# Performance work log

Hardware: AMD Instinct MI355X
Metric: run time of the kernel (lower is better)

The kernel has to match this reference:

```python
import jax, jax.numpy as jnp
import numpy as np

B, T, C = 4, 2048, 1024
H, HS = 16, 64  # n_heads, head_size; H*HS == C


def setup_inputs() -> dict:
    key = jax.random.key(0)
    ks = jax.random.split(key, 6)
    s = 0.02
    x = jax.random.normal(ks[0], (B, T, C), dtype=jnp.float32)
    Wq = jax.random.normal(ks[1], (H, C, HS), dtype=jnp.float32) * s
    Wk = jax.random.normal(ks[2], (H, C, HS), dtype=jnp.float32) * s
    Wv = jax.random.normal(ks[3], (H, C, HS), dtype=jnp.float32) * s
    Wo = jax.random.normal(ks[4], (C, C), dtype=jnp.float32) * s
    bo = jnp.zeros((C,), dtype=jnp.float32)
    return {"x": x, "Wq": Wq, "Wk": Wk, "Wv": Wv, "Wo": Wo, "bo": bo}


def reference(x, Wq, Wk, Wv, Wo, bo):
    # batched multi-head causal attention (math identical to per-head loop)
    q = jnp.einsum('btc,hcd->bhtd', x, Wq)  # [B,H,T,HS]
    k = jnp.einsum('btc,hcd->bhtd', x, Wk)
    v = jnp.einsum('btc,hcd->bhtd', x, Wv)
    scale = 1.0 / jnp.sqrt(jnp.asarray(HS, x.dtype))
    scores = jnp.einsum('bhtd,bhsd->bhts', q, k) * scale  # [B,H,T,T]
    causal = jnp.tril(jnp.ones((T, T), dtype=bool))
    scores = jnp.where(causal, scores, jnp.asarray(-jnp.inf, scores.dtype))
    attn = jax.nn.softmax(scores, axis=-1)
    out = jnp.einsum('bhts,bhsd->bhtd', attn, v)  # [B,H,T,HS]
    # concat heads along feature dim (head order == module list order)
    out = out.transpose(0, 2, 1, 3).reshape(B, T, C)
    return out @ Wo.T + bo
```

## Files before the change

### kernel.cpp

```cpp
#include <hip/hip_runtime.h>

typedef __attribute__((ext_vector_type(8))) short v8s;
typedef __attribute__((ext_vector_type(4))) short v4s;
typedef __attribute__((ext_vector_type(4))) float v4f;

static __device__ __forceinline__ short f2bf(float f) {
  union { float f; unsigned u; } c; c.f = f;
  unsigned r = c.u + 0x7fffu + ((c.u >> 16) & 1u);
  return (short)(r >> 16);
}

static __device__ __forceinline__ unsigned pk_bf16(float a, float b) {
  union { float f; unsigned u; } ca, cb; ca.f = a; cb.f = b;
  return ((ca.u + 0x8000u) >> 16) | ((cb.u + 0x8000u) & 0xffff0000u);
}

#if __has_builtin(__builtin_amdgcn_exp2f)
#define EXP2(x) __builtin_amdgcn_exp2f(x)
#else
#define EXP2(x) exp2f(x)
#endif

#define GLDS(gp, lp) __builtin_amdgcn_global_load_lds( \
    (const __attribute__((address_space(1))) void*)(gp), \
    (__attribute__((address_space(3))) void*)(lp), 16, 0, 0)


__global__ __launch_bounds__(256) void prep(const float* __restrict__ x,
                                            const float* __restrict__ Wq,
                                            const float* __restrict__ Wk,
                                            const float* __restrict__ Wv,
                                            const float* __restrict__ Wo,
                                            short* __restrict__ Xb,
                                            short* __restrict__ Wot,
                                            short* __restrict__ Wt) {
  __shared__ float tile[64][65];
  const int blk = blockIdx.x;
  const int tid = threadIdx.x;
  if (blk < 9216) {
    const float* src = (blk < 8192) ? x : Wo;
    short* dst = (blk < 8192) ? Xb : Wot;
    const int b2 = (blk < 8192) ? blk : (blk - 8192);
    const int idx = (b2 * 256 + tid) * 4;
    float4 v = *(const float4*)(src + idx);
    v4s o; o.x = f2bf(v.x); o.y = f2bf(v.y); o.z = f2bf(v.z); o.w = f2bf(v.w);
    *(v4s*)(dst + idx) = o;
    return;
  }
  const int bb = blk - 9216;
  const int sel = bb >> 8, rest = bb & 255;
  const int h = rest >> 4, kt = rest & 15;
  const float* W = (sel == 0) ? Wq : ((sel == 1) ? Wk : Wv);
  const int k0 = kt * 64;
  for (int i = 0; i < 4; ++i) {
    int c = i * 256 + tid;
    int row = c >> 4, c4 = (c & 15) * 4;
    float4 v = *(const float4*)(W + (size_t)h * 65536 + (size_t)(k0 + row) * 64 + c4);
    tile[row][c4 + 0] = v.x; tile[row][c4 + 1] = v.y;
    tile[row][c4 + 2] = v.z; tile[row][c4 + 3] = v.w;
  }
  __syncthreads();
  for (int i = 0; i < 2; ++i) {
    int c = i * 256 + tid;
    int d = c >> 3, k8 = (c & 7) * 8;
    v8s o;
    for (int j = 0; j < 8; ++j) o[j] = f2bf(tile[k8 + j][d]);
    *(v8s*)(Wt + (size_t)(sel * 1024 + h * 64 + d) * 1024 + k0 + k8) = o;
  }
}


#define GQ_STAGE_A(P, T) do {                                                     \
  _Pragma("unroll") for (int i_ = 0; i_ < 4; ++i_)                                \
    GLDS(Xb + (size_t)(m0 + rA + i_ * 64) * 1024 + (T) * 64 + cbl * 8,            \
         lds + (P) * 16384 + (tid + i_ * 512) * 8); } while (0)

#define GQ_STAGE_B(P, T) do {                                                     \
  _Pragma("unroll") for (int i_ = 0; i_ < 2; ++i_)                                \
    GLDS(Wt + (size_t)(n0 + rA + i_ * 64) * 1024 + (T) * 64 + cbl * 8,            \
         lds + 49152 + (P) * 8192 + (tid + i_ * 512) * 8); } while (0)

__global__ __launch_bounds__(512) void gemm_qkv(const short* __restrict__ Xb,
                                                const short* __restrict__ Wt,
                                                short* __restrict__ Qo,
                                                short* __restrict__ Ko,
                                                short* __restrict__ Vt) {
  __shared__ short lds[73728];
  const int tid = threadIdx.x;
  const int lane = tid & 63, quad = lane >> 4, l16 = lane & 15;
  const int wave = tid >> 6;
  const int m0 = blockIdx.x * 256, n0 = blockIdx.y * 128;
  const int wm = (wave >> 1) * 64, wn = (wave & 1) * 64;

  const int rA = tid >> 3;
  const int cbl = (tid & 7) ^ (rA & 7);

  const int swz = l16 & 7;
  const int csw0 = (quad ^ swz) * 8;
  const int csw1 = ((4 + quad) ^ swz) * 8;
  int aoff[4], boff[4];
#pragma unroll
  for (int mt = 0; mt < 4; ++mt) aoff[mt] = (wm + mt * 16 + l16) * 64;
#pragma unroll
  for (int nt = 0; nt < 4; ++nt) boff[nt] = (wn + nt * 16 + l16) * 64;

  v4f acc[4][4];
#pragma unroll
  for (int i = 0; i < 4; ++i)
#pragma unroll
    for (int j = 0; j < 4; ++j) acc[i][j] = (v4f){0.f, 0.f, 0.f, 0.f};

  GQ_STAGE_A(0, 0); GQ_STAGE_B(0, 0);
  GQ_STAGE_A(1, 1); GQ_STAGE_B(1, 1);
  asm volatile("s_waitcnt vmcnt(6)" ::: "memory");
  __builtin_amdgcn_s_barrier();

  int p = 0, pn = 2;
#pragma unroll 1
  for (int t = 0; t < 16; ++t) {
    int tn = t + 2; if (tn > 15) tn = 15;
    const short* lAp = lds + p * 16384;
    const short* lBp = lds + 49152 + p * 8192;

    GQ_STAGE_A(pn, tn);
    v8s a[4], b[4];
#pragma unroll
    for (int mt = 0; mt < 4; ++mt) a[mt] = *(const v8s*)(lAp + aoff[mt] + csw0);
#pragma unroll
    for (int nt = 0; nt < 4; ++nt) b[nt] = *(const v8s*)(lBp + boff[nt] + csw0);
    __builtin_amdgcn_s_setprio(1);
#pragma unroll
    for (int mt = 0; mt < 4; ++mt)
#pragma unroll
      for (int nt = 0; nt < 4; ++nt)
        acc[mt][nt] = __builtin_amdgcn_mfma_f32_16x16x32_bf16(a[mt], b[nt], acc[mt][nt], 0, 0, 0);
    __builtin_amdgcn_s_setprio(0);

    GQ_STAGE_B(pn, tn);
#pragma unroll
    for (int mt = 0; mt < 4; ++mt) a[mt] = *(const v8s*)(lAp + aoff[mt] + csw1);
#pragma unroll
    for (int nt = 0; nt < 4; ++nt) b[nt] = *(const v8s*)(lBp + boff[nt] + csw1);
    __builtin_amdgcn_s_setprio(1);
#pragma unroll
    for (int mt = 0; mt < 4; ++mt)
#pragma unroll
      for (int nt = 0; nt < 4; ++nt)
        acc[mt][nt] = __builtin_amdgcn_mfma_f32_16x16x32_bf16(a[mt], b[nt], acc[mt][nt], 0, 0, 0);
    __builtin_amdgcn_s_setprio(0);

    asm volatile("s_waitcnt vmcnt(6) lgkmcnt(0)" ::: "memory");
    __builtin_amdgcn_s_barrier();
    p = (p == 2) ? 0 : p + 1;
    pn = (pn == 2) ? 0 : pn + 1;
  }
  asm volatile("s_waitcnt vmcnt(0)" ::: "memory");

  const int selu = n0 >> 10;
  if (selu < 2) {
    short* obase = (selu == 0) ? Qo : Ko;
    const float sc = (selu == 0) ? 0.18033688011112042f : 1.0f;
#pragma unroll
    for (int nt = 0; nt < 4; ++nt) {
      int n = (n0 + wn + nt * 16 + l16) & 1023;
      int h = n >> 6, d = n & 63;
#pragma unroll
      for (int mt = 0; mt < 4; ++mt) {
        int m = m0 + wm + mt * 16 + quad * 4;
        int b_ = m >> 11, tt_ = m & 2047;
        size_t base = (size_t)((b_ * 16 + h) * 2048 + tt_) * 64 + d;
#pragma unroll
        for (int r = 0; r < 4; ++r)
          obase[base + (size_t)r * 64] = f2bf(acc[mt][nt][r] * sc);
      }
    }
  } else {
#pragma unroll
    for (int nt = 0; nt < 4; ++nt) {
      int n = (n0 + wn + nt * 16 + l16) & 1023;
      int h = n >> 6, d = n & 63;
#pragma unroll
      for (int mt = 0; mt < 4; ++mt) {
        int m = m0 + wm + mt * 16 + quad * 4;
        int b_ = m >> 11, tt_ = m & 2047;
        int2 dw;
        dw.x = (int)pk_bf16(acc[mt][nt][0], acc[mt][nt][1]);
        dw.y = (int)pk_bf16(acc[mt][nt][2], acc[mt][nt][3]);
        *(int2*)(Vt + ((size_t)(b_ * 16 + h) * 64 + d) * 2048 + tt_) = dw;
      }
    }
  }
}


#define ASTAGE(P, KB)                                                             \
  GLDS(K + qkbase + (size_t)((KB) + r0) * 64 + cl0 * 8, lK + (P) * 4096 + tid * 8);          \
  GLDS(K + qkbase + (size_t)((KB) + r1) * 64 + cl1 * 8, lK + (P) * 4096 + tid * 8 + 2048);   \
  GLDS(Vt + vtbase + (size_t)r0 * 2048 + (KB) + cl0 * 8, lV + (P) * 4096 + tid * 8);         \
  GLDS(Vt + vtbase + (size_t)r1 * 2048 + (KB) + cl1 * 8, lV + (P) * 4096 + tid * 8 + 2048)

__global__ __launch_bounds__(256, 2) void attn(const short* __restrict__ Q,
                                               const short* __restrict__ K,
                                               const short* __restrict__ Vt,
                                               short* __restrict__ AO) {
  __shared__ short lK[2 * 64 * 64];
  __shared__ short lV[2 * 64 * 64];
  __shared__ short lP[4 * 16 * 64];
  const int tid = threadIdx.x;
  const int w = tid >> 6, lane = tid & 63, quad = lane >> 4, l16 = lane & 15;
  const int bh = blockIdx.x & 63;
  const int slot = blockIdx.x >> 6;
  const int c = (int)((0x5410672398DCABEFull >> (slot * 4)) & 15ull);
  const unsigned psel = 0x07060302u;
  short* pw = lP + w * 1024;
  const size_t qkbase = (size_t)bh * 2048 * 64;
  const size_t vtbase = (size_t)bh * 64 * 2048;
  const int b_ = bh >> 4, h = bh & 15;

  const int r0 = tid >> 3, cp = tid & 7;
  const int cl0 = cp ^ (r0 & 7);
  const int r1 = r0 + 32;
  const int cl1 = cp ^ (r1 & 7);

  const int swz = l16 & 7;
  const int ph0 = (quad ^ swz) * 8;
  const int ph1 = ((quad + 4) ^ swz) * 8;

  const int qc = c * 128 + w * 32;

  v8s bQ[2][2];
#pragma unroll
  for (int qs = 0; qs < 2; ++qs) {
    const short* qb = Q + qkbase + (size_t)(qc + qs * 16 + l16) * 64 + quad * 8;
    bQ[qs][0] = *(const v8s*)(qb);
    bQ[qs][1] = *(const v8s*)(qb + 32);
  }
  v4f accO[2][4];
#pragma unroll
  for (int qs = 0; qs < 2; ++qs)
#pragma unroll
    for (int g = 0; g < 4; ++g) accO[qs][g] = (v4f){0.f, 0.f, 0.f, 0.f};
  float lrun[2] = {0.f, 0.f};

  const int nst = 2 * c + 2;

  ASTAGE(0, 0);

  for (int kt = 0; kt < nst; ++kt) {
    const int p = kt & 1;
    const int kb = kt * 64;
    if (kt + 1 < nst) {
      ASTAGE(p ^ 1, kb + 64);
      asm volatile("s_waitcnt vmcnt(4)" ::: "memory");
    } else {
      asm volatile("s_waitcnt vmcnt(0)" ::: "memory");
    }
    __builtin_amdgcn_s_barrier();
    const short* lKp = lK + p * 4096;
    const short* lVp = lV + p * 4096;

    const bool act0 = kb < qc + 16;
    const bool act1 = kb < qc + 32;
    if (act1) {
      v4f sT[2][4];
      {
        v8s aK[4][2];
#pragma unroll
        for (int mt = 0; mt < 4; ++mt) {
          const short* kr = lKp + (mt * 16 + l16) * 64;
          aK[mt][0] = *(const v8s*)(kr + ph0);
          aK[mt][1] = *(const v8s*)(kr + ph1);
        }
        __builtin_amdgcn_s_setprio(1);
#pragma unroll
        for (int qs = 0; qs < 2; ++qs) {
          if (qs == 0 ? !act0 : false) continue;
#pragma unroll
          for (int mt = 0; mt < 4; ++mt) {
            v4f t = (v4f){0.f, 0.f, 0.f, 0.f};
            t = __builtin_amdgcn_mfma_f32_16x16x32_bf16(aK[mt][0], bQ[qs][0], t, 0, 0, 0);
            t = __builtin_amdgcn_mfma_f32_16x16x32_bf16(aK[mt][1], bQ[qs][1], t, 0, 0, 0);
            sT[qs][mt] = t;
          }
        }
        __builtin_amdgcn_s_setprio(0);
      }
      v8s aV[4][2];
#pragma unroll
      for (int g = 0; g < 4; ++g) {
        const short* vr = lVp + (g * 16 + l16) * 64;
        aV[g][0] = *(const v8s*)(vr + ph0);
        aV[g][1] = *(const v8s*)(vr + ph1);
      }
#pragma unroll
      for (int qs = 0; qs < 2; ++qs) {
        if (qs == 0 ? !act0 : false) continue;
        const int rbase = qc + qs * 16;
        if (kb + 63 >= rbase) {
          const int kq = kb + quad * 4 - (rbase + l16);
#pragma unroll
          for (int mt = 0; mt < 4; ++mt)
#pragma unroll
            for (int r = 0; r < 4; ++r)
              if (kq + mt * 16 + r > 0) sT[qs][mt][r] = -__builtin_inff();
        }
        float ls = lrun[qs];
#pragma unroll
        for (int mt = 0; mt < 4; ++mt) {
          float p0 = EXP2(sT[qs][mt][0]);
          float p1 = EXP2(sT[qs][mt][1]);
          float p2 = EXP2(sT[qs][mt][2]);
          float p3 = EXP2(sT[qs][mt][3]);
          ls += (p0 + p1) + (p2 + p3);
          int2 dw;
          dw.x = (int)__builtin_amdgcn_perm(__float_as_uint(p1), __float_as_uint(p0), psel);
          dw.y = (int)__builtin_amdgcn_perm(__float_as_uint(p3), __float_as_uint(p2), psel);
          *(int2*)&pw[l16 * 64 + ((mt * 16 + quad * 4) ^ (swz * 8))] = dw;
        }
        lrun[qs] = ls;
        v8s bP0 = *(const v8s*)&pw[l16 * 64 + ph0];
        v8s bP1 = *(const v8s*)&pw[l16 * 64 + ph1];
        __builtin_amdgcn_s_setprio(1);
#pragma unroll
        for (int g = 0; g < 4; ++g) {
          accO[qs][g] = __builtin_amdgcn_mfma_f32_16x16x32_bf16(aV[g][0], bP0, accO[qs][g], 0, 0, 0);
          accO[qs][g] = __builtin_amdgcn_mfma_f32_16x16x32_bf16(aV[g][1], bP1, accO[qs][g], 0, 0, 0);
        }
        __builtin_amdgcn_s_setprio(0);
      }
    }
    __builtin_amdgcn_s_barrier();
  }

#pragma unroll
  for (int qs = 0; qs < 2; ++qs) {
    float ls = lrun[qs];
    ls += __shfl_xor(ls, 16);
    ls += __shfl_xor(ls, 32);
    float inv = __builtin_amdgcn_rcpf(ls);
    int t = qc + qs * 16 + l16;
    short* ao = AO + ((size_t)(b_ * 2048 + t)) * 1024 + h * 64 + quad * 4;
#pragma unroll
    for (int g = 0; g < 4; ++g) {
      int2 dw;
      dw.x = (int)pk_bf16(accO[qs][g][0] * inv, accO[qs][g][1] * inv);
      dw.y = (int)pk_bf16(accO[qs][g][2] * inv, accO[qs][g][3] * inv);
      *(int2*)(ao + g * 16) = dw;
    }
  }
}

#undef ASTAGE


__global__ __launch_bounds__(512) void gemm_out(const short* __restrict__ AO,
                                                const short* __restrict__ Wot,
                                                const float* __restrict__ bo,
                                                float* __restrict__ out) {
  __shared__ short lds[49152];
  const int tid = threadIdx.x;
  const int lane = tid & 63, quad = lane >> 4, l16 = lane & 15;
  const int wave = tid >> 6;
  const int m0 = blockIdx.x * 256, n0 = blockIdx.y * 128;
  const int wm = (wave >> 1) * 64, wn = (wave & 1) * 64;

  const int r0 = tid >> 2, cbs = (tid & 3) ^ ((r0 >> 1) & 3);
  const size_t offA0 = (size_t)(m0 + r0) * 1024 + cbs * 8;
  const size_t offB0 = (size_t)(n0 + r0) * 1024 + cbs * 8;

  int aoff[4], boff[4];
#pragma unroll
  for (int mt = 0; mt < 4; ++mt) {
    int row = wm + mt * 16 + l16;
    aoff[mt] = row * 32 + (quad ^ ((row >> 1) & 3)) * 8;
  }
#pragma unroll
  for (int nt = 0; nt < 4; ++nt) {
    int row = wn + nt * 16 + l16;
    boff[nt] = row * 32 + (quad ^ ((row >> 1) & 3)) * 8;
  }

  v4f acc[4][4];
#pragma unroll
  for (int i = 0; i < 4; ++i)
#pragma unroll
    for (int j = 0; j < 4; ++j) acc[i][j] = (v4f){0.f, 0.f, 0.f, 0.f};

#pragma unroll
  for (int t = 0; t < 3; ++t) {
    GLDS(AO + offA0 + t * 32, lds + t * 8192 + tid * 8);
    GLDS(AO + offA0 + 131072 + t * 32, lds + t * 8192 + 4096 + tid * 8);
    GLDS(Wot + offB0 + t * 32, lds + 32768 + t * 4096 + tid * 8);
  }
  asm volatile("s_waitcnt vmcnt(6)" ::: "memory");
  __builtin_amdgcn_s_barrier();

#pragma unroll 4
  for (int t = 0; t < 32; ++t) {
    const int p = t & 3;
    int tn = t + 3; if (tn > 31) tn = 31;
    const int pn = (t + 3) & 3;
    const short* lAp = lds + p * 8192;
    const short* lBp = lds + 32768 + p * 4096;

    GLDS(AO + offA0 + tn * 32, lds + pn * 8192 + tid * 8);
    GLDS(AO + offA0 + 131072 + tn * 32, lds + pn * 8192 + 4096 + tid * 8);
    v8s a[4], b[2];
#pragma unroll
    for (int mt = 0; mt < 4; ++mt) a[mt] = *(const v8s*)(lAp + aoff[mt]);
    b[0] = *(const v8s*)(lBp + boff[0]);
    b[1] = *(const v8s*)(lBp + boff[1]);
    __builtin_amdgcn_s_setprio(1);
#pragma unroll
    for (int mt = 0; mt < 4; ++mt) {
      acc[mt][0] = __builtin_amdgcn_mfma_f32_16x16x32_bf16(a[mt], b[0], acc[mt][0], 0, 0, 0);
      acc[mt][1] = __builtin_amdgcn_mfma_f32_16x16x32_bf16(a[mt], b[1], acc[mt][1], 0, 0, 0);
    }
    __builtin_amdgcn_s_setprio(0);

    GLDS(Wot + offB0 + tn * 32, lds + 32768 + pn * 4096 + tid * 8);
    b[0] = *(const v8s*)(lBp + boff[2]);
    b[1] = *(const v8s*)(lBp + boff[3]);
    __builtin_amdgcn_s_setprio(1);
#pragma unroll
    for (int mt = 0; mt < 4; ++mt) {
      acc[mt][2] = __builtin_amdgcn_mfma_f32_16x16x32_bf16(a[mt], b[0], acc[mt][2], 0, 0, 0);
      acc[mt][3] = __builtin_amdgcn_mfma_f32_16x16x32_bf16(a[mt], b[1], acc[mt][3], 0, 0, 0);
    }
    __builtin_amdgcn_s_setprio(0);

    asm volatile("s_waitcnt vmcnt(6) lgkmcnt(0)" ::: "memory");
    __builtin_amdgcn_s_barrier();
  }

#pragma unroll
  for (int nt = 0; nt < 4; ++nt) {
    int n = n0 + wn + nt * 16 + l16;
    float bias = bo[n];
#pragma unroll
    for (int mt = 0; mt < 4; ++mt) {
      int m = m0 + wm + mt * 16 + quad * 4;
#pragma unroll
      for (int r = 0; r < 4; ++r)
        out[(size_t)(m + r) * 1024 + n] = acc[mt][nt][r] + bias;
    }
  }
}


extern "C" void kernel_launch(void* const* d_in, const int* in_sizes, int n_in,
                              void* d_out, int out_size, void* d_ws, size_t ws_size,
                              hipStream_t stream) {
  const float* x  = (const float*)d_in[0];
  const float* Wq = (const float*)d_in[1];
  const float* Wk = (const float*)d_in[2];
  const float* Wv = (const float*)d_in[3];
  const float* Wo = (const float*)d_in[4];
  const float* bo = (const float*)d_in[5];
  float* out = (float*)d_out;
  char* ws = (char*)d_ws;

  short* Xb  = (short*)(ws);
  short* Wt  = (short*)(ws + (16u << 20));
  short* Wot = (short*)(ws + (22u << 20));
  short* Q   = (short*)(ws + (24u << 20));
  short* K   = (short*)(ws + (40u << 20));
  short* Vt  = (short*)(ws + (56u << 20));

  prep<<<9984, 256, 0, stream>>>(x, Wq, Wk, Wv, Wo, Xb, Wot, Wt);
  gemm_qkv<<<dim3(32, 24), 512, 0, stream>>>(Xb, Wt, Q, K, Vt);
  attn<<<1024, 256, 0, stream>>>(Q, K, Vt, Xb);
  gemm_out<<<dim3(32, 8), 512, 0, stream>>>(Xb, Wot, bo, out);
}
```

Before: 236.0 us.

## Restructure output GEMM to 64-wide K tiles with 3-stage buffering

The output-projection GEMM now loads 64-element K slices per stage instead of 32, with a 3-deep LDS ring (up from 4 stages of 32), an 8-way XOR swizzle, and a 16-iteration loop. This halves the barrier and loop overhead per unit of K and doubles the MFMA work between syncs, at the cost of more LDS per block (about 144 KB), which may reduce occupancy. The attention kernel's wait and barrier are also moved so each iteration drains all loads at its end rather than partially waiting at the start, which may serialize the prefetch more.

```diff
diff --git a/kernel.cpp b/kernel.cpp
--- a/kernel.cpp
+++ b/kernel.cpp
@@ -245,17 +245,15 @@
   const int nst = 2 * c + 2;
 
   ASTAGE(0, 0);
+  asm volatile("s_waitcnt vmcnt(0)" ::: "memory");
+  __builtin_amdgcn_s_barrier();
 
   for (int kt = 0; kt < nst; ++kt) {
     const int p = kt & 1;
     const int kb = kt * 64;
     if (kt + 1 < nst) {
       ASTAGE(p ^ 1, kb + 64);
-      asm volatile("s_waitcnt vmcnt(4)" ::: "memory");
-    } else {
-      asm volatile("s_waitcnt vmcnt(0)" ::: "memory");
-    }
-    __builtin_amdgcn_s_barrier();
+    }
     const short* lKp = lK + p * 4096;
     const short* lVp = lV + p * 4096;
 
@@ -329,6 +327,7 @@
         __builtin_amdgcn_s_setprio(0);
       }
     }
+    asm volatile("s_waitcnt vmcnt(0)" ::: "memory");
     __builtin_amdgcn_s_barrier();
   }
 
@@ -353,32 +352,38 @@
 #undef ASTAGE
 
 
+#define GO_STAGE_A(P, T) do {                                                     \
+  _Pragma("unroll") for (int i_ = 0; i_ < 4; ++i_)                                \
+    GLDS(AO + (size_t)(m0 + rA + i_ * 64) * 1024 + (T) * 64 + cbl * 8,            \
+         lds + (P) * 16384 + (tid + i_ * 512) * 8); } while (0)
+
+#define GO_STAGE_B(P, T) do {                                                     \
+  _Pragma("unroll") for (int i_ = 0; i_ < 2; ++i_)                                \
+    GLDS(Wot + (size_t)(n0 + rA + i_ * 64) * 1024 + (T) * 64 + cbl * 8,           \
+         lds + 49152 + (P) * 8192 + (tid + i_ * 512) * 8); } while (0)
+
 __global__ __launch_bounds__(512) void gemm_out(const short* __restrict__ AO,
                                                 const short* __restrict__ Wot,
                                                 const float* __restrict__ bo,
                                                 float* __restrict__ out) {
-  __shared__ short lds[49152];
+  __shared__ short lds[73728];
   const int tid = threadIdx.x;
   const int lane = tid & 63, quad = lane >> 4, l16 = lane & 15;
   const int wave = tid >> 6;
   const int m0 = blockIdx.x * 256, n0 = blockIdx.y * 128;
   const int wm = (wave >> 1) * 64, wn = (wave & 1) * 64;
 
-  const int r0 = tid >> 2, cbs = (tid & 3) ^ ((r0 >> 1) & 3);
-  const size_t offA0 = (size_t)(m0 + r0) * 1024 + cbs * 8;
-  const size_t offB0 = (size_t)(n0 + r0) * 1024 + cbs * 8;
-
+  const int rA = tid >> 3;
+  const int cbl = (tid & 7) ^ (rA & 7);
+
+  const int swz = l16 & 7;
+  const int csw0 = (quad ^ swz) * 8;
+  const int csw1 = ((4 + quad) ^ swz) * 8;
   int aoff[4], boff[4];
 #pragma unroll
-  for (int mt = 0; mt < 4; ++mt) {
-    int row = wm + mt * 16 + l16;
-    aoff[mt] = row * 32 + (quad ^ ((row >> 1) & 3)) * 8;
-  }
-#pragma unroll
-  for (int nt = 0; nt < 4; ++nt) {
-    int row = wn + nt * 16 + l16;
-    boff[nt] = row * 32 + (quad ^ ((row >> 1) & 3)) * 8;
-  }
+  for (int mt = 0; mt < 4; ++mt) aoff[mt] = (wm + mt * 16 + l16) * 64;
+#pragma unroll
+  for (int nt = 0; nt < 4; ++nt) boff[nt] = (wn + nt * 16 + l16) * 64;
 
   v4f acc[4][4];
 #pragma unroll
@@ -386,52 +391,51 @@
 #pragma unroll
     for (int j = 0; j < 4; ++j) acc[i][j] = (v4f){0.f, 0.f, 0.f, 0.f};
 
-#pragma unroll
-  for (int t = 0; t < 3; ++t) {
-    GLDS(AO + offA0 + t * 32, lds + t * 8192 + tid * 8);
-    GLDS(AO + offA0 + 131072 + t * 32, lds + t * 8192 + 4096 + tid * 8);
-    GLDS(Wot + offB0 + t * 32, lds + 32768 + t * 4096 + tid * 8);
-  }
+  GO_STAGE_A(0, 0); GO_STAGE_B(0, 0);
+  GO_STAGE_A(1, 1); GO_STAGE_B(1, 1);
   asm volatile("s_waitcnt vmcnt(6)" ::: "memory");
   __builtin_amdgcn_s_barrier();
 
-#pragma unroll 4
-  for (int t = 0; t < 32; ++t) {
-    const int p = t & 3;
-    int tn = t + 3; if (tn > 31) tn = 31;
-    const int pn = (t + 3) & 3;
-    const short* lAp = lds + p * 8192;
-    const short* lBp = lds + 32768 + p * 4096;
-
-    GLDS(AO + offA0 + tn * 32, lds + pn * 8192 + tid * 8);
-    GLDS(AO + offA0 + 131072 + tn * 32, lds + pn * 8192 + 4096 + tid * 8);
-    v8s a[4], b[2];
-#pragma unroll
-    for (int mt = 0; mt < 4; ++mt) a[mt] = *(const v8s*)(lAp + aoff[mt]);
-    b[0] = *(const v8s*)(lBp + boff[0]);
-    b[1] = *(const v8s*)(lBp + boff[1]);
+  int p = 0, pn = 2;
+#pragma unroll 1
+  for (int t = 0; t < 16; ++t) {
+    int tn = t + 2; if (tn > 15) tn = 15;
+    const short* lAp = lds + p * 16384;
+    const short* lBp = lds + 49152 + p * 8192;
+
+    GO_STAGE_A(pn, tn);
+    v8s a[4], b[4];
+#pragma unroll
+    for (int mt = 0; mt < 4; ++mt) a[mt] = *(const v8s*)(lAp + aoff[mt] + csw0);
+#pragma unroll
+    for (int nt = 0; nt < 4; ++nt) b[nt] = *(const v8s*)(lBp + boff[nt] + csw0);
     __builtin_amdgcn_s_setprio(1);
 #pragma unroll
-    for (int mt = 0; mt < 4; ++mt) {
-      acc[mt][0] = __builtin_amdgcn_mfma_f32_16x16x32_bf16(a[mt], b[0], acc[mt][0], 0, 0, 0);
-      acc[mt][1] = __builtin_amdgcn_mfma_f32_16x16x32_bf16(a[mt], b[1], acc[mt][1], 0, 0, 0);
-    }
+    for (int mt = 0; mt < 4; ++mt)
+#pragma unroll
+      for (int nt = 0; nt < 4; ++nt)
+        acc[mt][nt] = __builtin_amdgcn_mfma_f32_16x16x32_bf16(a[mt], b[nt], acc[mt][nt], 0, 0, 0);
     __builtin_amdgcn_s_setprio(0);
 
-    GLDS(Wot + offB0 + tn * 32, lds + 32768 + pn * 4096 + tid * 8);
-    b[0] = *(const v8s*)(lBp + boff[2]);
-    b[1] = *(const v8s*)(lBp + boff[3]);
+    GO_STAGE_B(pn, tn);
+#pragma unroll
+    for (int mt = 0; mt < 4; ++mt) a[mt] = *(const v8s*)(lAp + aoff[mt] + csw1);
+#pragma unroll
+    for (int nt = 0; nt < 4; ++nt) b[nt] = *(const v8s*)(lBp + boff[nt] + csw1);
     __builtin_amdgcn_s_setprio(1);
 #pragma unroll
-    for (int mt = 0; mt < 4; ++mt) {
-      acc[mt][2] = __builtin_amdgcn_mfma_f32_16x16x32_bf16(a[mt], b[0], acc[mt][2], 0, 0, 0);
-      acc[mt][3] = __builtin_amdgcn_mfma_f32_16x16x32_bf16(a[mt], b[1], acc[mt][3], 0, 0, 0);
-    }
+    for (int mt = 0; mt < 4; ++mt)
+#pragma unroll
+      for (int nt = 0; nt < 4; ++nt)
+        acc[mt][nt] = __builtin_amdgcn_mfma_f32_16x16x32_bf16(a[mt], b[nt], acc[mt][nt], 0, 0, 0);
     __builtin_amdgcn_s_setprio(0);
 
     asm volatile("s_waitcnt vmcnt(6) lgkmcnt(0)" ::: "memory");
     __builtin_amdgcn_s_barrier();
-  }
+    p = (p == 2) ? 0 : p + 1;
+    pn = (pn == 2) ? 0 : pn + 1;
+  }
+  asm volatile("s_waitcnt vmcnt(0)" ::: "memory");
 
 #pragma unroll
   for (int nt = 0; nt < 4; ++nt) {
```

New measurement: 228.7 us. 3.1% less time.
